# Performance work log

Hardware: AMD Instinct MI355X
Metric: run time of the kernel (lower is better)

## Reference

```python
import jax, jax.numpy as jnp
import numpy as np
from jax import lax

TOPK = 10
THRESHOLD = 0.5
MARGIN = 0.5
EPS = 1e-8


def setup_inputs() -> dict:
    key = jax.random.key(0)
    k1, k2 = jax.random.split(key)
    B, C, H, W = 8, 256, 128, 128
    loc_features = jax.random.normal(k1, (B, C, H, W), dtype=jnp.float32)
    det_features = jax.random.normal(k2, (B, C, H, W), dtype=jnp.float32)
    return {"loc_features": loc_features, "det_features": det_features}


def _peak_features(fmap):
    """fmap: [C,H,W] -> (feats [TOPK,C], valid [TOPK] bool).
    Peaks = pixels equal to their 3x3 local max with intensity > THRESHOLD,
    sorted by intensity descending, top TOPK (padded with invalid slots)."""
    C, H, W = fmap.shape
    intensity = jnp.sqrt(jnp.sum(fmap * fmap, axis=0))  # [H,W] L2 norm over channels
    pooled = lax.reduce_window(intensity, -jnp.inf, lax.max,
                               (3, 3), (1, 1), 'SAME')
    peak_mask = (intensity == pooled) & (intensity > THRESHOLD)
    masked = jnp.where(peak_mask, intensity, -jnp.inf).reshape(-1)  # [H*W]
    vals, idx = lax.top_k(masked, TOPK)
    valid = jnp.isfinite(vals)  # slots beyond the actual peak count are -inf
    y = idx // W
    x = idx % W
    feats = fmap[:, y, x].T  # [TOPK, C]
    return feats, valid


def _cosine_sim(a, b):
    # a: [Ka,C], b: [Kb,C]; torch.cosine_similarity semantics with eps clamp
    na = jnp.maximum(jnp.linalg.norm(a, axis=-1), EPS)  # [Ka]
    nb = jnp.maximum(jnp.linalg.norm(b, axis=-1), EPS)  # [Kb]
    return (a @ b.T) / (na[:, None] * nb[None, :])


def _per_sample_loss(det_map, loc_map):
    det_f, det_v = _peak_features(det_map)
    loc_f, loc_v = _peak_features(loc_map)
    sim = _cosine_sim(det_f, loc_f)  # [TOPK, TOPK]
    pair_mask = det_v[:, None] & loc_v[None, :]
    n_pairs = jnp.sum(pair_mask)
    loss_sum = jnp.sum(jnp.where(pair_mask, jax.nn.relu(sim - MARGIN), 0.0))
    # torch 'continue' when either side has no peaks -> contributes 0
    return jnp.where(n_pairs > 0, loss_sum / jnp.maximum(n_pairs, 1).astype(sim.dtype), 0.0)


def reference(loc_features, det_features):
    B = loc_features.shape[0]
    losses = jax.vmap(_per_sample_loss)(det_features, loc_features)  # [B]
    return jnp.sum(losses) / B
```

## Files before the change

### kernel.cpp

```cpp
#include <hip/hip_runtime.h>
#include <math.h>

namespace {
constexpr int kB = 8;
constexpr int kC = 256;
constexpr int kH = 128;
constexpr int kW = 128;
constexpr int kHW = kH * kW;
constexpr int kTopK = 10;
constexpr float kThreshold = 0.5f;
constexpr float kMargin = 0.5f;
constexpr float kEps = 1e-8f;
constexpr int kMaps = 2 * kB;
constexpr int kChunks = 8;
constexpr int kCPer = kC / kChunks;
constexpr int kSegs = 16;
constexpr int kSegPx = kHW / kSegs;
}

__global__ __launch_bounds__(256, 8) void sumsq_kernel(
    const float* __restrict__ loc, const float* __restrict__ det,
    float* __restrict__ partial) {
  const int bid = blockIdx.x;
  const int m = bid >> 7;
  const int r = bid & 127;
  const int ch = r >> 4;
  const int seg = r & 15;
  const int t = threadIdx.x;
  const float* __restrict__ src = (m < kB) ? loc : det;
  const int b = m & (kB - 1);
  const float* base = src + (size_t)b * kC * kHW +
                      (size_t)(ch * kCPer) * kHW + seg * kSegPx + t * 4;
  float4 acc = {0.f, 0.f, 0.f, 0.f};
  for (int c0 = 0; c0 < kCPer; c0 += 8) {
    float4 v[8];
#pragma unroll
    for (int j = 0; j < 8; ++j)
      v[j] = *(const float4*)(base + (size_t)(c0 + j) * kHW);
#pragma unroll
    for (int j = 0; j < 8; ++j) {
      acc.x = fmaf(v[j].x, v[j].x, acc.x);
      acc.y = fmaf(v[j].y, v[j].y, acc.y);
      acc.z = fmaf(v[j].z, v[j].z, acc.z);
      acc.w = fmaf(v[j].w, v[j].w, acc.w);
    }
  }
  *(float4*)(partial + ((size_t)ch * kMaps + m) * kHW + seg * kSegPx +
             t * 4) = acc;
}

__global__ __launch_bounds__(256) void combine_kernel(
    const float* __restrict__ partial, float* __restrict__ inten) {
  const int g = blockIdx.x * 256 + threadIdx.x;
  const int m = g >> 12;
  const int p = (g & 4095) * 4;
  const float* pp = partial + (size_t)m * kHW + p;
  float4 s = *(const float4*)(pp);
#pragma unroll
  for (int ch = 1; ch < kChunks; ++ch) {
    const float4 q = *(const float4*)(pp + (size_t)ch * kMaps * kHW);
    s.x += q.x; s.y += q.y; s.z += q.z; s.w += q.w;
  }
  float4 o = {sqrtf(s.x), sqrtf(s.y), sqrtf(s.z), sqrtf(s.w)};
  *(float4*)(inten + (size_t)m * kHW + p) = o;
}

__global__ __launch_bounds__(1024) void topk_kernel(
    const float* __restrict__ inten, float* __restrict__ tvals,
    int* __restrict__ tidx) {
  const int m = blockIdx.x;
  const int t = threadIdx.x;
  const float* __restrict__ I = inten + (size_t)m * kHW;

  float v[16];
#pragma unroll
  for (int k = 0; k < 16; ++k) {
    const int p = k * 1024 + t;
    const int y = p >> 7;
    const int x = p & (kW - 1);
    const float c0 = I[p];
    float nmax = -INFINITY;
    for (int dy = -1; dy <= 1; ++dy) {
      const int yy = y + dy;
      if (yy < 0 || yy >= kH) continue;
      for (int dx = -1; dx <= 1; ++dx) {
        const int xx = x + dx;
        if (xx < 0 || xx >= kW) continue;
        nmax = fmaxf(nmax, I[yy * kW + xx]);
      }
    }
    const bool peak = (c0 > kThreshold) && (c0 >= nmax);
    v[k] = peak ? c0 : -INFINITY;
  }

  __shared__ float s_wv[16];
  __shared__ int s_wi[16];
  __shared__ int s_bi;
  const int wave = t >> 6;
  const int lane = t & 63;

  for (int r = 0; r < kTopK; ++r) {
    float bv = v[0];
    int bi = t;
#pragma unroll
    for (int k = 1; k < 16; ++k) {
      const int idx = k * 1024 + t;
      if (v[k] > bv || (v[k] == bv && idx < bi)) { bv = v[k]; bi = idx; }
    }
    for (int off = 32; off > 0; off >>= 1) {
      const float ov = __shfl_down(bv, off, 64);
      const int oi = __shfl_down(bi, off, 64);
      if (ov > bv || (ov == bv && oi < bi)) { bv = ov; bi = oi; }
    }
    if (lane == 0) { s_wv[wave] = bv; s_wi[wave] = bi; }
    __syncthreads();
    if (t == 0) {
      float xv = s_wv[0];
      int xi = s_wi[0];
      for (int w2 = 1; w2 < 16; ++w2) {
        if (s_wv[w2] > xv || (s_wv[w2] == xv && s_wi[w2] < xi)) {
          xv = s_wv[w2];
          xi = s_wi[w2];
        }
      }
      s_bi = xi;
      tvals[m * kTopK + r] = xv;
      tidx[m * kTopK + r] = xi;
    }
    __syncthreads();
    const int wi = s_bi;
    if ((wi & 1023) == t) v[wi >> 10] = -INFINITY;
    __syncthreads();
  }
}

__global__ __launch_bounds__(256) void loss_kernel(
    const float* __restrict__ loc, const float* __restrict__ det,
    const float* __restrict__ tvals, const int* __restrict__ tidx,
    float* __restrict__ losses) {
  const int b = blockIdx.x;
  const int t = threadIdx.x;
  __shared__ float ds[kTopK][kC + 1];
  __shared__ float ls[kTopK][kC + 1];
  __shared__ float s_red[kC];

  float lv[kTopK], dv[kTopK];
  int li[kTopK], di[kTopK];
#pragma unroll
  for (int i = 0; i < kTopK; ++i) {
    lv[i] = tvals[b * kTopK + i];
    li[i] = tidx[b * kTopK + i];
    dv[i] = tvals[(kB + b) * kTopK + i];
    di[i] = tidx[(kB + b) * kTopK + i];
  }
  const float* lb = loc + (size_t)b * kC * kHW + (size_t)t * kHW;
  const float* db = det + (size_t)b * kC * kHW + (size_t)t * kHW;
#pragma unroll
  for (int i = 0; i < kTopK; ++i) {
    ls[i][t] = lb[li[i]];
    ds[i][t] = db[di[i]];
  }
  __syncthreads();

  float contrib = 0.f;
  if (t < kTopK * kTopK) {
    const int i = t / kTopK;
    const int j = t % kTopK;
    const bool valid = (dv[i] > -1e30f) && (lv[j] > -1e30f);
    if (valid) {
      float dot = 0.f;
#pragma unroll 8
      for (int c = 0; c < kC; ++c) dot = fmaf(ds[i][c], ls[j][c], dot);
      const float na = fmaxf(dv[i], kEps);
      const float nb = fmaxf(lv[j], kEps);
      const float sim = dot / (na * nb);
      contrib = fmaxf(sim - kMargin, 0.f);
    }
  }
  s_red[t] = contrib;
  __syncthreads();
  if (t == 0) {
    int nd = 0, nl = 0;
    for (int i = 0; i < kTopK; ++i) {
      nd += (dv[i] > -1e30f) ? 1 : 0;
      nl += (lv[i] > -1e30f) ? 1 : 0;
    }
    float s = 0.f;
    for (int k = 0; k < kTopK * kTopK; ++k) s += s_red[k];
    const int np = nd * nl;
    losses[b] = (np > 0) ? (s / (float)np) : 0.f;
  }
}

__global__ void final_kernel(const float* __restrict__ losses,
                             float* __restrict__ out) {
  if (threadIdx.x == 0 && blockIdx.x == 0) {
    float s = 0.f;
    for (int i = 0; i < kB; ++i) s += losses[i];
    out[0] = s / (float)kB;
  }
}

extern "C" void kernel_launch(void* const* d_in, const int* in_sizes, int n_in,
                              void* d_out, int out_size, void* d_ws,
                              size_t ws_size, hipStream_t stream) {
  const float* loc = (const float*)d_in[0];
  const float* det = (const float*)d_in[1];
  float* out = (float*)d_out;

  float* wsf = (float*)d_ws;
  float* partial = wsf;
  float* inten = partial + (size_t)kChunks * kMaps * kHW;
  float* tvals = inten + (size_t)kMaps * kHW;
  int* tidx = (int*)(tvals + kMaps * kTopK);
  float* losses = (float*)(tidx + kMaps * kTopK);

  sumsq_kernel<<<dim3(kMaps * kChunks * kSegs), dim3(256), 0, stream>>>(
      loc, det, partial);
  combine_kernel<<<dim3(kMaps * kHW / 4 / 256), dim3(256), 0, stream>>>(
      partial, inten);
  topk_kernel<<<dim3(kMaps), dim3(1024), 0, stream>>>(inten, tvals, tidx);
  loss_kernel<<<dim3(kB), dim3(kC), 0, stream>>>(loc, det, tvals, tidx,
                                                 losses);
  final_kernel<<<dim3(1), dim3(64), 0, stream>>>(losses, out);
}
```

Before: 357.4 us.

## Restructure sum-of-squares with LDS accumulators and sync-free per-wave top-k

The sum-of-squares kernel now assigns each 512-thread block one map and a group of 16 channel planes. It reads each full 64 KB plane contiguously and accumulates into a 64 KB LDS buffer, emitting 16 partials per map instead of 8. The intent is more contiguous streaming with larger loads in flight. The cost is occupancy limited by LDS, extra LDS traffic, and double the partial writes and reads in combine. The top-k kernel now has each wave find its own top 10 with xor shuffles and no block barriers, then a single wave merges the 160 candidates.

```diff
diff --git a/kernel.cpp b/kernel.cpp
--- a/kernel.cpp
+++ b/kernel.cpp
@@ -12,54 +12,77 @@
 constexpr float kMargin = 0.5f;
 constexpr float kEps = 1e-8f;
 constexpr int kMaps = 2 * kB;
-constexpr int kChunks = 8;
-constexpr int kCPer = kC / kChunks;
-constexpr int kSegs = 16;
-constexpr int kSegPx = kHW / kSegs;
-}
-
-__global__ __launch_bounds__(256, 8) void sumsq_kernel(
+constexpr int kGrpPlanes = 16;
+constexpr int kGroups = kC / kGrpPlanes;
+}
+
+__global__ __launch_bounds__(512) void sumsq_kernel(
     const float* __restrict__ loc, const float* __restrict__ det,
     float* __restrict__ partial) {
+  __shared__ float acc[kHW];
   const int bid = blockIdx.x;
-  const int m = bid >> 7;
-  const int r = bid & 127;
-  const int ch = r >> 4;
-  const int seg = r & 15;
+  const int m = bid >> 4;
+  const int g = bid & 15;
   const int t = threadIdx.x;
+  const int w = t >> 6;
+  const int lane = t & 63;
   const float* __restrict__ src = (m < kB) ? loc : det;
   const int b = m & (kB - 1);
   const float* base = src + (size_t)b * kC * kHW +
-                      (size_t)(ch * kCPer) * kHW + seg * kSegPx + t * 4;
-  float4 acc = {0.f, 0.f, 0.f, 0.f};
-  for (int c0 = 0; c0 < kCPer; c0 += 8) {
+                      (size_t)(g * kGrpPlanes) * kHW + w * 2048 + lane * 4;
+  float* lacc = acc + w * 2048 + lane * 4;
+
+  {
     float4 v[8];
 #pragma unroll
-    for (int j = 0; j < 8; ++j)
-      v[j] = *(const float4*)(base + (size_t)(c0 + j) * kHW);
-#pragma unroll
-    for (int j = 0; j < 8; ++j) {
-      acc.x = fmaf(v[j].x, v[j].x, acc.x);
-      acc.y = fmaf(v[j].y, v[j].y, acc.y);
-      acc.z = fmaf(v[j].z, v[j].z, acc.z);
-      acc.w = fmaf(v[j].w, v[j].w, acc.w);
-    }
-  }
-  *(float4*)(partial + ((size_t)ch * kMaps + m) * kHW + seg * kSegPx +
-             t * 4) = acc;
+    for (int i = 0; i < 8; ++i) v[i] = *(const float4*)(base + i * 256);
+    __builtin_amdgcn_sched_barrier(0);
+#pragma unroll
+    for (int i = 0; i < 8; ++i) {
+      float4 o;
+      o.x = v[i].x * v[i].x;
+      o.y = v[i].y * v[i].y;
+      o.z = v[i].z * v[i].z;
+      o.w = v[i].w * v[i].w;
+      *(float4*)(lacc + i * 256) = o;
+    }
+  }
+  for (int j = 1; j < kGrpPlanes; ++j) {
+    const float* pb = base + (size_t)j * kHW;
+    float4 v[8];
+#pragma unroll
+    for (int i = 0; i < 8; ++i) v[i] = *(const float4*)(pb + i * 256);
+    __builtin_amdgcn_sched_barrier(0);
+#pragma unroll
+    for (int i = 0; i < 8; ++i) {
+      float4 a = *(const float4*)(lacc + i * 256);
+      a.x = fmaf(v[i].x, v[i].x, a.x);
+      a.y = fmaf(v[i].y, v[i].y, a.y);
+      a.z = fmaf(v[i].z, v[i].z, a.z);
+      a.w = fmaf(v[i].w, v[i].w, a.w);
+      *(float4*)(lacc + i * 256) = a;
+    }
+  }
+  float* out = partial + ((size_t)m * kGroups + g) * kHW + w * 2048 + lane * 4;
+#pragma unroll
+  for (int i = 0; i < 8; ++i)
+    *(float4*)(out + i * 256) = *(const float4*)(lacc + i * 256);
 }
 
 __global__ __launch_bounds__(256) void combine_kernel(
     const float* __restrict__ partial, float* __restrict__ inten) {
-  const int g = blockIdx.x * 256 + threadIdx.x;
-  const int m = g >> 12;
-  const int p = (g & 4095) * 4;
-  const float* pp = partial + (size_t)m * kHW + p;
-  float4 s = *(const float4*)(pp);
-#pragma unroll
-  for (int ch = 1; ch < kChunks; ++ch) {
-    const float4 q = *(const float4*)(pp + (size_t)ch * kMaps * kHW);
-    s.x += q.x; s.y += q.y; s.z += q.z; s.w += q.w;
+  const int gi = blockIdx.x * 256 + threadIdx.x;
+  const int m = gi >> 12;
+  const int p = (gi & 4095) * 4;
+  const float* pp = partial + (size_t)m * kGroups * kHW + p;
+  float4 s = {0.f, 0.f, 0.f, 0.f};
+#pragma unroll
+  for (int g = 0; g < kGroups; ++g) {
+    const float4 q = *(const float4*)(pp + (size_t)g * kHW);
+    s.x += q.x;
+    s.y += q.y;
+    s.z += q.z;
+    s.w += q.w;
   }
   float4 o = {sqrtf(s.x), sqrtf(s.y), sqrtf(s.z), sqrtf(s.w)};
   *(float4*)(inten + (size_t)m * kHW + p) = o;
@@ -70,6 +93,8 @@
     int* __restrict__ tidx) {
   const int m = blockIdx.x;
   const int t = threadIdx.x;
+  const int w = t >> 6;
+  const int lane = t & 63;
   const float* __restrict__ I = inten + (size_t)m * kHW;
 
   float v[16];
@@ -93,12 +118,8 @@
     v[k] = peak ? c0 : -INFINITY;
   }
 
-  __shared__ float s_wv[16];
-  __shared__ int s_wi[16];
-  __shared__ int s_bi;
-  const int wave = t >> 6;
-  const int lane = t & 63;
-
+  __shared__ float swv[16][kTopK];
+  __shared__ int swi[16][kTopK];
   for (int r = 0; r < kTopK; ++r) {
     float bv = v[0];
     int bi = t;
@@ -107,30 +128,49 @@
       const int idx = k * 1024 + t;
       if (v[k] > bv || (v[k] == bv && idx < bi)) { bv = v[k]; bi = idx; }
     }
-    for (int off = 32; off > 0; off >>= 1) {
-      const float ov = __shfl_down(bv, off, 64);
-      const int oi = __shfl_down(bi, off, 64);
+    for (int off = 1; off < 64; off <<= 1) {
+      const float ov = __shfl_xor(bv, off, 64);
+      const int oi = __shfl_xor(bi, off, 64);
       if (ov > bv || (ov == bv && oi < bi)) { bv = ov; bi = oi; }
     }
-    if (lane == 0) { s_wv[wave] = bv; s_wi[wave] = bi; }
-    __syncthreads();
-    if (t == 0) {
-      float xv = s_wv[0];
-      int xi = s_wi[0];
-      for (int w2 = 1; w2 < 16; ++w2) {
-        if (s_wv[w2] > xv || (s_wv[w2] == xv && s_wi[w2] < xi)) {
-          xv = s_wv[w2];
-          xi = s_wi[w2];
-        }
-      }
-      s_bi = xi;
-      tvals[m * kTopK + r] = xv;
-      tidx[m * kTopK + r] = xi;
-    }
-    __syncthreads();
-    const int wi = s_bi;
-    if ((wi & 1023) == t) v[wi >> 10] = -INFINITY;
-    __syncthreads();
+    if (lane == r) { swv[w][r] = bv; swi[w][r] = bi; }
+    if ((bi & 1023) == t) v[bi >> 10] = -INFINITY;
+  }
+  __syncthreads();
+
+  if (w == 0) {
+    float cv[3];
+    int ci[3];
+#pragma unroll
+    for (int q = 0; q < 3; ++q) {
+      const int s = lane + 64 * q;
+      if (s < 16 * kTopK) {
+        cv[q] = swv[s / kTopK][s % kTopK];
+        ci[q] = swi[s / kTopK][s % kTopK];
+      } else {
+        cv[q] = -INFINITY;
+        ci[q] = 0x7fffffff;
+      }
+    }
+    for (int r = 0; r < kTopK; ++r) {
+      float bv = cv[0];
+      int bi = ci[0];
+#pragma unroll
+      for (int q = 1; q < 3; ++q)
+        if (cv[q] > bv || (cv[q] == bv && ci[q] < bi)) { bv = cv[q]; bi = ci[q]; }
+      for (int off = 1; off < 64; off <<= 1) {
+        const float ov = __shfl_xor(bv, off, 64);
+        const int oi = __shfl_xor(bi, off, 64);
+        if (ov > bv || (ov == bv && oi < bi)) { bv = ov; bi = oi; }
+      }
+      if (lane == r) {
+        tvals[m * kTopK + r] = bv;
+        tidx[m * kTopK + r] = bi;
+      }
+#pragma unroll
+      for (int q = 0; q < 3; ++q)
+        if (ci[q] == bi) { cv[q] = -INFINITY; ci[q] = 0x7fffffff; }
+    }
   }
 }
 
@@ -210,13 +250,13 @@
 
   float* wsf = (float*)d_ws;
   float* partial = wsf;
-  float* inten = partial + (size_t)kChunks * kMaps * kHW;
+  float* inten = partial + (size_t)kMaps * kGroups * kHW;
   float* tvals = inten + (size_t)kMaps * kHW;
   int* tidx = (int*)(tvals + kMaps * kTopK);
   float* losses = (float*)(tidx + kMaps * kTopK);
 
-  sumsq_kernel<<<dim3(kMaps * kChunks * kSegs), dim3(256), 0, stream>>>(
-      loc, det, partial);
+  sumsq_kernel<<<dim3(kMaps * kGroups), dim3(512), 0, stream>>>(loc, det,
+                                                                partial);
   combine_kernel<<<dim3(kMaps * kHW / 4 / 256), dim3(256), 0, stream>>>(
       partial, inten);
   topk_kernel<<<dim3(kMaps), dim3(1024), 0, stream>>>(inten, tvals, tidx);
```

Result: faster. 345.1 us (-3.4%).
